# Kernel tuning notes

Measured on AMD Instinct MI355X. Metric: run time of the kernel, lower is better.

Reference implementation:

```python
import jax, jax.numpy as jnp
import numpy as np

EPS = 1e-12  # torch F.normalize default eps

def _l2_normalize(x):
    # F.normalize(x, dim=1): x / max(||x||_2, eps), per row
    n = jnp.linalg.norm(x, axis=1, keepdims=True)
    return x / jnp.maximum(n, EPS)

def setup_inputs() -> dict:
    key = jax.random.key(0)
    ks = jax.random.split(key, 7)
    B, D = 8192, 4096
    s = 1.0 / np.sqrt(D)  # keep activations well-scaled like nn.Linear init
    return {
        "x":  jax.random.normal(ks[0], (B, D), dtype=jnp.float32),
        "W0": jax.random.normal(ks[1], (D, D), dtype=jnp.float32) * s,
        "b0": jax.random.normal(ks[2], (D,),   dtype=jnp.float32) * s,
        "W1": jax.random.normal(ks[3], (D, D), dtype=jnp.float32) * s,
        "b1": jax.random.normal(ks[4], (D,),   dtype=jnp.float32) * s,
        "W2": jax.random.normal(ks[5], (D, D), dtype=jnp.float32) * s,
        "b2": jax.random.normal(ks[6], (D,),   dtype=jnp.float32) * s,
    }

def reference(x, W0, b0, W1, b1, W2, b2):
    # per layer: out = relu(Linear(l2_normalize(x, dim=1))); collect all layer outputs
    params = [(W0, b0), (W1, b1), (W2, b2)]
    outs = []
    h = x
    for W, b in params:
        hn = _l2_normalize(h)
        # nn.Linear stores weight as [out, in]: y = hn @ W.T + b
        h = jax.nn.relu(jnp.einsum('bi,oi->bo', hn, W) + b)
        outs.append(h)
    return tuple(outs)
```

## Files before the change

### kernel.cpp

```cpp
#include <hip/hip_runtime.h>
#include <hip/hip_bf16.h>


#define NROWS 8192
#define DIM   4096

typedef __bf16 bf16x8 __attribute__((ext_vector_type(8)));
typedef float  f32x4  __attribute__((ext_vector_type(4)));

__device__ static inline short f2bf(float f) {
  __hip_bfloat16 h = __float2bfloat16(f);
  return __builtin_bit_cast(short, h);
}

#define BARRIER() do { asm volatile("" ::: "memory"); \
                       __builtin_amdgcn_s_barrier();  \
                       asm volatile("" ::: "memory"); } while (0)
#define LGKM0()  asm volatile("s_waitcnt lgkmcnt(0)" ::: "memory")

__global__ __launch_bounds__(512, 2)
void gemm256_bias_relu(const short* __restrict__ A,
                       const short* __restrict__ Bw,
                       const float* __restrict__ bias,
                       float* __restrict__ C,
                       int M, int N, int K)
{
  __shared__ short lds[4][16384];

  int bid = blockIdx.x;
  const int nwg = gridDim.x;
  if ((nwg & 7) == 0) { const int cpx = nwg >> 3; bid = (bid & 7) * cpx + (bid >> 3); }
  const int nbn  = N >> 8;
  const int brow = (bid / nbn) << 8;
  const int bcol = (bid % nbn) << 8;

  const int lane = threadIdx.x & 63;
  const int wid  = threadIdx.x >> 6;
  const int wr   = wid >> 2;
  const int wc   = wid & 3;

  float bv[4];
#pragma unroll
  for (int j = 0; j < 4; ++j)
    bv[j] = bias[bcol + wc * 64 + j * 16 + (lane & 15)];

  f32x4 acc[8][4] = {};

  const size_t Kz   = (size_t)K;
  const size_t rowK = Kz * 2;
  const char*  Ag   = (const char*)A;
  const char*  Bg   = (const char*)Bw;
  char* const  ldsB = (char*)&lds[0][0];

  const int r8  = lane >> 3;
  const int kcs = (lane & 7) ^ r8;
  const size_t gAl = (size_t)(brow + r8) * rowK + (size_t)kcs * 16;
  const size_t gBl = (size_t)(bcol + r8) * rowK + (size_t)kcs * 16;

  auto stage_half = [&](int tile, int op, int h) {
    const char*  gp = op ? Bg : Ag;
    const size_t gt = (op ? gBl : gAl) + (size_t)tile * 128;
    char* lb = ldsB + ((tile & 1) * 2 + op) * 32768;
#pragma unroll
    for (int s = 0; s < 2; ++s) {
      const int rb = h * 128 + s * 64 + wid * 8;
      __builtin_amdgcn_global_load_lds(
          (const __attribute__((address_space(1))) void*)(gp + gt + (size_t)rb * rowK),
          (__attribute__((address_space(3))) void*)(lb + rb * 128), 16, 0, 0);
    }
  };

  const int l15  = lane & 15;
  const int xlo  = ((lane >> 4) ^ (lane & 3)) * 16;
  const int b2   = (lane >> 2) & 1;
  const int k64[2] = { b2 << 6, (1 - b2) << 6 };
  const int abase = (wr * 128 + l15) * 128 + xlo;
  const int bbase = (wc * 64  + l15) * 128 + xlo;

  const int NT = K >> 6;

  bf16x8 aS[2][2][2];
  bf16x8 bF[4][2];

#define LOAD_A(SET, I0, PTR)                                                 \
  _Pragma("unroll")                                                          \
  for (int ii = 0; ii < 2; ++ii)                                             \
    _Pragma("unroll")                                                        \
    for (int ks = 0; ks < 2; ++ks)                                           \
      aS[SET][ii][ks] = *reinterpret_cast<const bf16x8*>(                    \
          (PTR) + abase + ((I0) + ii) * 2048 + k64[ks]);

#define MFMA2(I0, SET)                                                       \
  _Pragma("unroll")                                                          \
  for (int ii = 0; ii < 2; ++ii)                                             \
    _Pragma("unroll")                                                        \
    for (int j = 0; j < 4; ++j)                                              \
      _Pragma("unroll")                                                      \
      for (int ks = 0; ks < 2; ++ks)                                         \
        acc[(I0) + ii][j] = __builtin_amdgcn_mfma_f32_16x16x32_bf16(         \
            aS[SET][ii][ks], bF[j][ks], acc[(I0) + ii][j], 0, 0, 0);

  stage_half(0, 0, 0); stage_half(0, 0, 1);
  stage_half(0, 1, 0); stage_half(0, 1, 1);
  if (NT > 1) { stage_half(1, 1, 0); stage_half(1, 1, 1); }
  if (NT > 1) asm volatile("s_waitcnt vmcnt(4)" ::: "memory");
  else        asm volatile("s_waitcnt vmcnt(0)" ::: "memory");
  BARRIER();
  {
    const char* A0 = ldsB;
    LOAD_A(0, 0, A0)
  }

  for (int t = 0; t < NT; ++t) {
    const char* At = ldsB + ((t & 1) * 2 + 0) * 32768;
    const char* Bt = ldsB + ((t & 1) * 2 + 1) * 32768;
    const char* An = ldsB + (((t + 1) & 1) * 2 + 0) * 32768;

    if (t + 1 < NT) stage_half(t + 1, 0, 0);
#pragma unroll
    for (int j = 0; j < 4; ++j)
#pragma unroll
      for (int ks = 0; ks < 2; ++ks)
        bF[j][ks] = *reinterpret_cast<const bf16x8*>(Bt + bbase + j * 2048 + k64[ks]);
    BARRIER();
    LGKM0();
    LOAD_A(1, 2, At)
    __builtin_amdgcn_s_setprio(1);
    MFMA2(0, 0)
    __builtin_amdgcn_s_setprio(0);
    BARRIER();

    if (t + 1 < NT) stage_half(t + 1, 0, 1);
    BARRIER();
    LGKM0();
    LOAD_A(0, 4, At)
    __builtin_amdgcn_s_setprio(1);
    MFMA2(2, 1)
    __builtin_amdgcn_s_setprio(0);
    BARRIER();

    if (t + 2 < NT) stage_half(t + 2, 1, 0);
    BARRIER();
    LGKM0();
    LOAD_A(1, 6, At)
    __builtin_amdgcn_s_setprio(1);
    MFMA2(4, 0)
    __builtin_amdgcn_s_setprio(0);
    BARRIER();

    if (t + 2 < NT) stage_half(t + 2, 1, 1);
    if (t >= NT - 2) asm volatile("s_waitcnt vmcnt(0)" ::: "memory");
    else             asm volatile("s_waitcnt vmcnt(4)" ::: "memory");
    BARRIER();
    LGKM0();
    if (t + 1 < NT) { LOAD_A(0, 0, An) }
    __builtin_amdgcn_s_setprio(1);
    MFMA2(6, 1)
    __builtin_amdgcn_s_setprio(0);
    BARRIER();
  }
#undef MFMA2
#undef LOAD_A

#pragma unroll
  for (int i = 0; i < 8; ++i) {
    const int rbase = brow + wr * 128 + i * 16 + ((lane >> 4) << 2);
#pragma unroll
    for (int j = 0; j < 4; ++j) {
      const int col = bcol + wc * 64 + j * 16 + (lane & 15);
#pragma unroll
      for (int r = 0; r < 4; ++r) {
        const float v = acc[i][j][r] + bv[j];
        C[(size_t)(rbase + r) * N + col] = v > 0.f ? v : 0.f;
      }
    }
  }
}

__global__ __launch_bounds__(256)
void rownorm_bf16(const float* __restrict__ in, short* __restrict__ out)
{
  const int row = blockIdx.x;
  const int t0  = threadIdx.x;
  const float4* inr = (const float4*)(in + (size_t)row * DIM);

  float4 v[4];
  float ss = 0.f;
#pragma unroll
  for (int t = 0; t < 4; ++t) {
    v[t] = inr[t0 + t * 256];
    ss += v[t].x * v[t].x + v[t].y * v[t].y + v[t].z * v[t].z + v[t].w * v[t].w;
  }
#pragma unroll
  for (int off = 32; off > 0; off >>= 1)
    ss += __shfl_down(ss, off, 64);

  __shared__ float wss[4];
  if ((t0 & 63) == 0) wss[t0 >> 6] = ss;
  __syncthreads();
  const float tot   = wss[0] + wss[1] + wss[2] + wss[3];
  const float scale = 1.f / fmaxf(sqrtf(tot), 1e-12f);

  short4* outr = (short4*)(out + (size_t)row * DIM);
#pragma unroll
  for (int t = 0; t < 4; ++t) {
    short4 o;
    o.x = f2bf(v[t].x * scale);
    o.y = f2bf(v[t].y * scale);
    o.z = f2bf(v[t].z * scale);
    o.w = f2bf(v[t].w * scale);
    outr[t0 + t * 256] = o;
  }
}

__global__ __launch_bounds__(256)
void cast_bf16(const float* __restrict__ in, short* __restrict__ out, int n4)
{
  int i = blockIdx.x * 256 + threadIdx.x;
  const int stride = gridDim.x * 256;
  for (; i < n4; i += stride) {
    const float4 v = ((const float4*)in)[i];
    short4 o;
    o.x = f2bf(v.x);
    o.y = f2bf(v.y);
    o.z = f2bf(v.z);
    o.w = f2bf(v.w);
    ((short4*)out)[i] = o;
  }
}

extern "C" void kernel_launch(void* const* d_in, const int* in_sizes, int n_in,
                              void* d_out, int out_size, void* d_ws, size_t ws_size,
                              hipStream_t stream) {
  const float* x = (const float*)d_in[0];
  const float* W[3]    = { (const float*)d_in[1], (const float*)d_in[3], (const float*)d_in[5] };
  const float* bias[3] = { (const float*)d_in[2], (const float*)d_in[4], (const float*)d_in[6] };
  float* out = (float*)d_out;

  short* hn = (short*)d_ws;
  short* Wb = (short*)((char*)d_ws + (size_t)NROWS * DIM * 2);

  const size_t layer_elems = (size_t)NROWS * DIM;
  const float* hin = x;

  for (int L = 0; L < 3; ++L) {
    cast_bf16<<<2048, 256, 0, stream>>>(W[L], Wb, DIM * DIM / 4);
    rownorm_bf16<<<NROWS, 256, 0, stream>>>(hin, hn);
    gemm256_bias_relu<<<(NROWS / 256) * (DIM / 256), 512, 0, stream>>>(
        hn, Wb, bias[L], out + (size_t)L * layer_elems, NROWS, DIM, DIM);
    hin = out + (size_t)L * layer_elems;
  }
}
```

Before: 868.7 us.

## Drop redundant GEMM barriers, precompute staging addresses, reorder MFMA loop nest

Removes several workgroup barriers per K-iteration of the 256x256 bf16 GEMM by merging staging phases and moving one A-fragment LDS read ahead of its barrier. Global and LDS staging offsets are now precomputed per thread rather than recomputed for each load. The MFMA nest is reordered so the k-slice loop is outermost, which spreads dependent accumulations apart. The aim is less barrier stall and address arithmetic in the main loop, at the cost of subtler hazard reasoning about LDS double-buffer reuse.

```diff
diff --git a/kernel.cpp b/kernel.cpp
--- a/kernel.cpp
+++ b/kernel.cpp
@@ -48,25 +48,30 @@
 
   const size_t Kz   = (size_t)K;
   const size_t rowK = Kz * 2;
-  const char*  Ag   = (const char*)A;
-  const char*  Bg   = (const char*)Bw;
   char* const  ldsB = (char*)&lds[0][0];
 
   const int r8  = lane >> 3;
   const int kcs = (lane & 7) ^ r8;
-  const size_t gAl = (size_t)(brow + r8) * rowK + (size_t)kcs * 16;
-  const size_t gBl = (size_t)(bcol + r8) * rowK + (size_t)kcs * 16;
-
-  auto stage_half = [&](int tile, int op, int h) {
-    const char*  gp = op ? Bg : Ag;
-    const size_t gt = (op ? gBl : gAl) + (size_t)tile * 128;
-    char* lb = ldsB + ((tile & 1) * 2 + op) * 32768;
+  const char* AgL = (const char*)A  + (size_t)(brow + r8) * rowK + (size_t)kcs * 16;
+  const char* BgL = (const char*)Bw + (size_t)(bcol + r8) * rowK + (size_t)kcs * 16;
+  size_t rbo[4];
+  int    rbb[4];
+#pragma unroll
+  for (int i = 0; i < 4; ++i) {
+    const int rb = wid * 8 + i * 64;
+    rbo[i] = (size_t)rb * rowK;
+    rbb[i] = rb * 128;
+  }
+
+  auto stage_half = [&](int parity, int op, int h, int tile) {
+    const char* gp = (op ? BgL : AgL) + ((size_t)tile << 7);
+    char* lb = ldsB + (parity * 2 + op) * 32768;
 #pragma unroll
     for (int s = 0; s < 2; ++s) {
-      const int rb = h * 128 + s * 64 + wid * 8;
+      const int idx = h * 2 + s;
       __builtin_amdgcn_global_load_lds(
-          (const __attribute__((address_space(1))) void*)(gp + gt + (size_t)rb * rowK),
-          (__attribute__((address_space(3))) void*)(lb + rb * 128), 16, 0, 0);
+          (const __attribute__((address_space(1))) void*)(gp + rbo[idx]),
+          (__attribute__((address_space(3))) void*)(lb + rbb[idx]), 16, 0, 0);
     }
   };
 
@@ -92,17 +97,17 @@
 
 #define MFMA2(I0, SET)                                                       \
   _Pragma("unroll")                                                          \
-  for (int ii = 0; ii < 2; ++ii)                                             \
+  for (int ks = 0; ks < 2; ++ks)                                             \
     _Pragma("unroll")                                                        \
-    for (int j = 0; j < 4; ++j)                                              \
+    for (int ii = 0; ii < 2; ++ii)                                           \
       _Pragma("unroll")                                                      \
-      for (int ks = 0; ks < 2; ++ks)                                         \
+      for (int j = 0; j < 4; ++j)                                            \
         acc[(I0) + ii][j] = __builtin_amdgcn_mfma_f32_16x16x32_bf16(         \
             aS[SET][ii][ks], bF[j][ks], acc[(I0) + ii][j], 0, 0, 0);
 
-  stage_half(0, 0, 0); stage_half(0, 0, 1);
-  stage_half(0, 1, 0); stage_half(0, 1, 1);
-  if (NT > 1) { stage_half(1, 1, 0); stage_half(1, 1, 1); }
+  stage_half(0, 0, 0, 0); stage_half(0, 0, 1, 0);
+  stage_half(0, 1, 0, 0); stage_half(0, 1, 1, 0);
+  if (NT > 1) { stage_half(1, 1, 0, 1); stage_half(1, 1, 1, 1); }
   if (NT > 1) asm volatile("s_waitcnt vmcnt(4)" ::: "memory");
   else        asm volatile("s_waitcnt vmcnt(0)" ::: "memory");
   BARRIER();
@@ -112,11 +117,12 @@
   }
 
   for (int t = 0; t < NT; ++t) {
-    const char* At = ldsB + ((t & 1) * 2 + 0) * 32768;
-    const char* Bt = ldsB + ((t & 1) * 2 + 1) * 32768;
-    const char* An = ldsB + (((t + 1) & 1) * 2 + 0) * 32768;
-
-    if (t + 1 < NT) stage_half(t + 1, 0, 0);
+    const int cur = t & 1, nxt = cur ^ 1;
+    const char* At = ldsB + (cur * 2 + 0) * 32768;
+    const char* Bt = ldsB + (cur * 2 + 1) * 32768;
+    const char* An = ldsB + (nxt * 2 + 0) * 32768;
+
+    if (t + 1 < NT) stage_half(nxt, 0, 0, t + 1);
 #pragma unroll
     for (int j = 0; j < 4; ++j)
 #pragma unroll
@@ -128,27 +134,24 @@
     __builtin_amdgcn_s_setprio(1);
     MFMA2(0, 0)
     __builtin_amdgcn_s_setprio(0);
-    BARRIER();
-
-    if (t + 1 < NT) stage_half(t + 1, 0, 1);
+
+    if (t + 1 < NT) stage_half(nxt, 0, 1, t + 1);
     BARRIER();
     LGKM0();
     LOAD_A(0, 4, At)
     __builtin_amdgcn_s_setprio(1);
     MFMA2(2, 1)
     __builtin_amdgcn_s_setprio(0);
-    BARRIER();
-
-    if (t + 2 < NT) stage_half(t + 2, 1, 0);
-    BARRIER();
-    LGKM0();
+
+    if (t + 2 < NT) stage_half(cur, 1, 0, t + 2);
     LOAD_A(1, 6, At)
+    BARRIER();
+    LGKM0();
     __builtin_amdgcn_s_setprio(1);
     MFMA2(4, 0)
     __builtin_amdgcn_s_setprio(0);
-    BARRIER();
-
-    if (t + 2 < NT) stage_half(t + 2, 1, 1);
+
+    if (t + 2 < NT) stage_half(cur, 1, 1, t + 2);
     if (t >= NT - 2) asm volatile("s_waitcnt vmcnt(0)" ::: "memory");
     else             asm volatile("s_waitcnt vmcnt(4)" ::: "memory");
     BARRIER();
@@ -157,7 +160,6 @@
     __builtin_amdgcn_s_setprio(1);
     MFMA2(6, 1)
     __builtin_amdgcn_s_setprio(0);
-    BARRIER();
   }
 #undef MFMA2
 #undef LOAD_A
```

Measured after the change: 797.9 us. 1.09x faster.
